# Performance work log

Hardware: AMD Instinct MI355X
Metric: run time of the kernel (lower is better)

## Reference

```python
import jax, jax.numpy as jnp
import numpy as np

N, E, C_IN, C_HID, C_OUT = 50000, 800000, 128, 128, 128


def _mlp2(x, w1, b1, w2, b2):
    # build_mlp: 2 layers, no layer norm, plain_last=False -> ReLU after both
    h = jax.nn.relu(x @ w1 + b1)
    return jax.nn.relu(h @ w2 + b2)


def setup_inputs() -> dict:
    key = jax.random.key(0)
    ks = jax.random.split(key, 16)
    s = 0.05
    inp = {
        "x": jax.random.normal(ks[0], (N, C_IN), jnp.float32),
        "pos": jax.random.normal(ks[1], (N, C_IN), jnp.float32),
        "edge_index": jax.random.randint(ks[2], (2, E), 0, N, jnp.int64),
        # lin_in (with bias)
        "W_in": jax.random.normal(ks[3], (C_IN, C_IN), jnp.float32) * s,
        "b_in": jnp.zeros((C_IN,), jnp.float32),
        # PointTransformerConv linear maps (bias=False in PyG)
        "W_lin": jax.random.normal(ks[4], (C_IN, C_OUT), jnp.float32) * s,
        "W_src": jax.random.normal(ks[5], (C_IN, C_OUT), jnp.float32) * s,
        "W_dst": jax.random.normal(ks[6], (C_IN, C_OUT), jnp.float32) * s,
        # pos_nn: in_channels -> hidden -> out_channels
        "pos_w1": jax.random.normal(ks[7], (C_IN, C_HID), jnp.float32) * s,
        "pos_b1": jnp.zeros((C_HID,), jnp.float32),
        "pos_w2": jax.random.normal(ks[8], (C_HID, C_OUT), jnp.float32) * s,
        "pos_b2": jnp.zeros((C_OUT,), jnp.float32),
        # attn_nn: out_channels -> hidden -> out_channels
        "att_w1": jax.random.normal(ks[9], (C_OUT, C_HID), jnp.float32) * s,
        "att_b1": jnp.zeros((C_HID,), jnp.float32),
        "att_w2": jax.random.normal(ks[10], (C_HID, C_OUT), jnp.float32) * s,
        "att_b2": jnp.zeros((C_OUT,), jnp.float32),
        # lin_out (with bias)
        "W_out": jax.random.normal(ks[11], (C_OUT, C_OUT), jnp.float32) * s,
        "b_out": jnp.zeros((C_OUT,), jnp.float32),
    }
    return inp


def reference(x, pos, edge_index, W_in, b_in, W_lin, W_src, W_dst,
              pos_w1, pos_b1, pos_w2, pos_b2,
              att_w1, att_b1, att_w2, att_b2, W_out, b_out):
    n = x.shape[0]
    src, dst = edge_index[0], edge_index[1]  # j -> i

    h = jax.nn.relu(x @ W_in + b_in)                 # [N, C_IN]
    q = h @ W_dst                                    # dest queries
    k = h @ W_src                                    # source keys
    v = h @ W_lin                                    # values

    delta = _mlp2(pos[dst] - pos[src], pos_w1, pos_b1, pos_w2, pos_b2)  # [E, C_OUT]
    alpha = _mlp2(q[dst] - k[src] + delta, att_w1, att_b1, att_w2, att_b2)

    # per-channel segment softmax over destination nodes
    m = jax.ops.segment_max(alpha, dst, num_segments=n)
    m = jnp.where(jnp.isfinite(m), m, 0.0)
    ea = jnp.exp(alpha - m[dst])
    z = jax.ops.segment_sum(ea, dst, num_segments=n)
    attn = ea / (z[dst] + 1e-16)

    msg = attn * (v[src] + delta)                    # [E, C_OUT]
    agg = jax.ops.segment_sum(msg, dst, num_segments=n)

    return jax.nn.relu(agg @ W_out + b_out)
```

## Files before the change

### kernel.cpp

```cpp
#include <hip/hip_runtime.h>
#include <hip/hip_bf16.h>

#define C 128
#define THREADS 256
#define ETHREADS 128
#define EWPB 2
#define TILE 64
#define EPW 16
#define GTILES 8
#define LDSPAD 8
#define LDSW (C + LDSPAD)
#define LOG2E 1.44269504088896340736f

typedef unsigned short ushortT;
typedef __attribute__((ext_vector_type(8))) short short8;
typedef __attribute__((ext_vector_type(8))) ushortT ushort8;
typedef __attribute__((ext_vector_type(4))) float floatx4;
typedef __attribute__((ext_vector_type(4))) unsigned uintx4;

__device__ __forceinline__ unsigned pk2(float a, float b) {
    float2 f; f.x = a; f.y = b;
    union { unsigned u; __hip_bfloat162 h; } cv; cv.h = __float22bfloat162_rn(f);
    return cv.u;
}
__device__ __forceinline__ ushortT f2bf(float x) {
    return (ushortT)(pk2(x, x) & 0xffffu);
}
__device__ __forceinline__ float bf2f(ushortT h) {
    union { unsigned u; float f; } v; v.u = ((unsigned)h) << 16;
    return v.f;
}
__device__ __forceinline__ float2 upk2(unsigned u) {
    union { unsigned u; __hip_bfloat162 h; } cv; cv.u = u;
    return __bfloat1622float2(cv.h);
}
__device__ __forceinline__ float exp2_hw(float x) {
    float r; asm("v_exp_f32 %0, %1" : "=v"(r) : "v"(x)); return r;
}
__device__ __forceinline__ void atomic_add_f32(float* p, float v) {
    __hip_atomic_fetch_add(p, v, __ATOMIC_RELAXED, __HIP_MEMORY_SCOPE_AGENT);
}

__device__ __forceinline__ void wave_gemm(const ushortT (*A)[LDSW],
                                          const ushortT* __restrict__ Bp,
                                          int quad, int m16, int lane,
                                          floatx4 acc[8])
{
#pragma unroll
    for (int nt = 0; nt < 8; ++nt) { acc[nt][0]=0.f; acc[nt][1]=0.f; acc[nt][2]=0.f; acc[nt][3]=0.f; }
#pragma unroll 1
    for (int ks = 0; ks < 4; ++ks) {
        const short8 af = *(const short8*)&A[m16][ks * 32 + quad * 8];
        const ushortT* bpk = Bp + (size_t)ks * 4096 + (size_t)lane * 8;
#pragma unroll
        for (int nt = 0; nt < 8; ++nt) {
            const short8 bf = *(const short8*)(bpk + nt * 512);
            acc[nt] = __builtin_amdgcn_mfma_f32_16x16x32_bf16(af, bf, acc[nt], 0, 0, 0);
        }
    }
}

__device__ __forceinline__ void cstore_relu_r(ushortT (*A)[LDSW], floatx4 acc[8],
                                              const float bias[8], int quad, int m16)
{
#pragma unroll
    for (int nt = 0; nt < 8; ++nt) {
        const float b = bias[nt];
#pragma unroll
        for (int r = 0; r < 4; r += 2) {
            const unsigned p = pk2(fmaxf(acc[nt][r] + b, 0.f), fmaxf(acc[nt][r + 1] + b, 0.f));
            A[quad * 4 + r][nt * 16 + m16]     = (ushortT)(p & 0xffffu);
            A[quad * 4 + r + 1][nt * 16 + m16] = (ushortT)(p >> 16);
        }
    }
}

__device__ __forceinline__ ushortT pack_one(const float* __restrict__ W, int u) {
    const int j = u & 7, lane = (u >> 3) & 63, f = u >> 9;
    const int nt = f & 7, ks = f >> 3;
    const int n = nt * 16 + (lane & 15);
    const int k = ks * 32 + (lane >> 4) * 8 + j;
    return f2bf(W[k * C + n]);
}

extern "C" __global__ void __launch_bounds__(256)
prep1(const float* __restrict__ pw1, const float* __restrict__ pw2,
      const float* __restrict__ aw1, const float* __restrict__ aw2,
      const float* __restrict__ Wd,  const float* __restrict__ Wsrc,
      const float* __restrict__ Wl,  const float* __restrict__ Win,
      const float* __restrict__ Wout,
      const float* __restrict__ pos, ushortT* __restrict__ pos_bf,
      const int* __restrict__ ei, int* __restrict__ deg,
      ushortT* __restrict__ Bpack, ushortT* __restrict__ Bpack2,
      ushortT* __restrict__ BpackO, int N, int E)
{
    const int nb_cvt = (N * 32 + 255) / 256;
    const int b = blockIdx.x, tid = threadIdx.x;
    if (b < 256) {
        const int t = b * 256 + tid;
        const int s = t >> 14;
        const float* W = (s == 0) ? pw1 : (s == 1) ? pw2 : (s == 2) ? aw1 : aw2;
        const int u = t & 16383;
        const int j = u & 7, lane = (u >> 3) & 63, f = u >> 9;
        const int nt = f & 7, ks = f >> 3;
        const int n = nt * 16 + (lane & 15);
        const int k = ks * 32 + (lane >> 4) * 8 + j;
        float v = W[k * C + n];
        if (s == 3) v *= LOG2E;
        Bpack[t] = f2bf(v);
    } else if (b < 512) {
        const int t = (b - 256) * 256 + tid;
        const int s = t >> 14;
        const float* W = (s == 0) ? Wd : (s == 1) ? Wsrc : (s == 2) ? Wl : Win;
        Bpack2[t] = pack_one(W, t & 16383);
    } else if (b < 576) {
        const int t = (b - 512) * 256 + tid;
        BpackO[t] = pack_one(Wout, t);
    } else if (b < 576 + nb_cvt) {
        const int i = (b - 576) * 256 + tid;
        if (i < N * 32) {
            const float4 v = ((const float4*)pos)[i];
            uint2 o; o.x = pk2(v.x, v.y); o.y = pk2(v.z, v.w);
            ((uint2*)pos_bf)[i] = o;
        }
    } else {
        const int e = (b - 576 - nb_cvt) * 256 + tid;
        if (e < E) atomicAdd(&deg[ei[E + e]], 1);
    }
}

extern "C" __global__ void __launch_bounds__(1024)
k_scan(const int* __restrict__ deg, int* __restrict__ off, int n)
{
    __shared__ int part[1024];
    const int t = threadIdx.x;
    const int chunk = (((n + 1023) / 1024) + 3) & ~3;
    const int lo = t * chunk, hi = min(lo + chunk, n);
    int s = 0;
    for (int i = lo; i < hi; i += 4) {
        const int4 d4 = *(const int4*)(deg + i);
        s += d4.x + d4.y + d4.z + d4.w;
    }
    part[t] = s;
    __syncthreads();
    for (int d = 1; d < 1024; d <<= 1) {
        int v = (t >= d) ? part[t - d] : 0;
        __syncthreads();
        part[t] += v;
        __syncthreads();
    }
    int run = (t == 0) ? 0 : part[t - 1];
    for (int i = lo; i < hi; i += 4) {
        const int4 d4 = *(const int4*)(deg + i);
        int4 o;
        o.x = run;
        o.y = o.x + d4.x;
        o.z = o.y + d4.y;
        o.w = o.z + d4.z;
        *(int4*)(off + i) = o;
        run = o.w + d4.w;
    }
}

extern "C" __global__ void __launch_bounds__(256)
prep2(const float* __restrict__ x, const float* __restrict__ b_in,
      const ushortT* __restrict__ Bp2, const ushortT* __restrict__ Bpk,
      const float* __restrict__ pb1, const ushortT* __restrict__ pos_bf,
      ushortT* __restrict__ q_bf, ushortT* __restrict__ k_bf, ushortT* __restrict__ v_bf,
      ushortT* __restrict__ Pd_arr, ushortT* __restrict__ Ps_arr,
      const int* __restrict__ ei, const int* __restrict__ offp, int* __restrict__ curp,
      int* __restrict__ ss, int* __restrict__ sd, int N, int E, int nb_node)
{
    __shared__ ushortT xs[TILE][LDSW];
    __shared__ ushortT hs[TILE][LDSW];
    const int b = blockIdx.x, tx = threadIdx.x;

    if (b >= nb_node) {
        const int e = (b - nb_node) * 256 + tx;
        if (e < E) {
            const int d = ei[E + e];
            const int p = offp[d] + atomicAdd(&curp[d], 1);
            ss[p] = ei[e];
            sd[p] = d;
        }
        return;
    }

    const int rg = tx >> 5;
    const int oc0 = (tx & 31) << 2;
    const int row0 = b * TILE;

#pragma unroll
    for (int j = 0; j < 8; ++j) {
        const int r = rg * 8 + j, n = row0 + r;
        float4 xv; xv.x = xv.y = xv.z = xv.w = 0.f;
        if (n < N) xv = *(const float4*)(x + (size_t)n * C + oc0);
        *(unsigned*)&xs[r][oc0]     = pk2(xv.x, xv.y);
        *(unsigned*)&xs[r][oc0 + 2] = pk2(xv.z, xv.w);
    }

    const int wv = tx >> 6, lane = tx & 63;
    const int quad = lane >> 4, m16 = lane & 15;
    const int row = lane >> 2, li = lane & 3;

    float binv[8];
#pragma unroll
    for (int nt = 0; nt < 8; ++nt) binv[nt] = b_in[nt * 16 + m16];

    const ushortT (*Ax)[LDSW] = (const ushortT (*)[LDSW])&xs[wv * 16];
    ushortT (*Ah)[LDSW] = (ushortT (*)[LDSW])&hs[wv * 16];

    floatx4 macc[8];
    wave_gemm(Ax, Bp2 + (size_t)3 * 16384, quad, m16, lane, macc);
    cstore_relu_r(Ah, macc, binv, quad, m16);

    __syncthreads();

    ushortT (*OS)[LDSW] = (ushortT (*)[LDSW])&xs[wv * 16];
    ushortT* outs[3];
    outs[0] = q_bf; outs[1] = k_bf; outs[2] = v_bf;

    const int nrow = row0 + wv * 16 + row;

#pragma unroll 1
    for (int m = 0; m < 3; ++m) {
        wave_gemm((const ushortT (*)[LDSW])Ah, Bp2 + (size_t)m * 16384, quad, m16, lane, macc);
#pragma unroll
        for (int nt = 0; nt < 8; ++nt) {
#pragma unroll
            for (int r = 0; r < 4; r += 2) {
                const unsigned p = pk2(macc[nt][r], macc[nt][r + 1]);
                OS[quad * 4 + r][nt * 16 + m16]     = (ushortT)(p & 0xffffu);
                OS[quad * 4 + r + 1][nt * 16 + m16] = (ushortT)(p >> 16);
            }
        }
        if (nrow < N) {
#pragma unroll
            for (int i = 0; i < 4; ++i) {
                const ushort8 v8 = *(const ushort8*)&OS[row][i * 32 + li * 8];
                *(ushort8*)(outs[m] + (size_t)nrow * C + i * 32 + li * 8) = v8;
            }
        }
    }

    __syncthreads();
    {
        const ushortT* srcp = pos_bf + (size_t)min(nrow, N - 1) * C;
#pragma unroll
        for (int i = 0; i < 4; ++i) {
            const ushort8 v8 = *(const ushort8*)(srcp + i * 32 + li * 8);
            *(ushort8*)&hs[wv * 16 + row][i * 32 + li * 8] = v8;
        }
    }
    __syncthreads();
    wave_gemm((const ushortT (*)[LDSW])Ah, Bpk , quad, m16, lane, macc);

    float b1v[8];
#pragma unroll
    for (int nt = 0; nt < 8; ++nt) b1v[nt] = pb1[nt * 16 + m16];

#pragma unroll
    for (int nt = 0; nt < 8; ++nt) {
#pragma unroll
        for (int r = 0; r < 4; r += 2) {
            const unsigned p = pk2(macc[nt][r] + b1v[nt], macc[nt][r + 1] + b1v[nt]);
            OS[quad * 4 + r][nt * 16 + m16]     = (ushortT)(p & 0xffffu);
            OS[quad * 4 + r + 1][nt * 16 + m16] = (ushortT)(p >> 16);
        }
    }
    if (nrow < N) {
#pragma unroll
        for (int i = 0; i < 4; ++i) {
            const ushort8 v8 = *(const ushort8*)&OS[row][i * 32 + li * 8];
            *(ushort8*)(Pd_arr + (size_t)nrow * C + i * 32 + li * 8) = v8;
        }
    }
    __syncthreads();
#pragma unroll
    for (int nt = 0; nt < 8; ++nt) {
#pragma unroll
        for (int r = 0; r < 4; r += 2) {
            const unsigned p = pk2(macc[nt][r], macc[nt][r + 1]);
            OS[quad * 4 + r][nt * 16 + m16]     = (ushortT)(p & 0xffffu);
            OS[quad * 4 + r + 1][nt * 16 + m16] = (ushortT)(p >> 16);
        }
    }
    if (nrow < N) {
#pragma unroll
        for (int i = 0; i < 4; ++i) {
            const ushort8 v8 = *(const ushort8*)&OS[row][i * 32 + li * 8];
            *(ushort8*)(Ps_arr + (size_t)nrow * C + i * 32 + li * 8) = v8;
        }
    }
}

__device__ __forceinline__ void gather4(const ushortT* __restrict__ base, int node, int li,
                                        ushort8 dst[4])
{
    const ushort8* p = (const ushort8*)(base + (size_t)node * C) + li;
    dst[0] = p[0]; dst[1] = p[4]; dst[2] = p[8]; dst[3] = p[12];
}

extern "C" __global__ void __launch_bounds__(ETHREADS)
edge_mfma(const ushortT* __restrict__ Pd_arr, const ushortT* __restrict__ Ps_arr,
          const int* __restrict__ ss, const int* __restrict__ sd,
          const ushortT* __restrict__ q_bf, const ushortT* __restrict__ k_bf,
          const ushortT* __restrict__ v_bf, const ushortT* __restrict__ Bpack,
          const float* __restrict__ pb2,
          const float* __restrict__ ab1, const float* __restrict__ ab2,
          float* __restrict__ z, float* __restrict__ aggU, int E)
{
    __shared__ ushortT Aslab[EWPB][EPW][LDSW];
    __shared__ ushortT Vslab[EWPB][EPW][LDSW];
    __shared__ int     Dslab[EWPB][EPW];
    const int tid = threadIdx.x;
    const int wv = tid >> 6, lane = tid & 63;
    const int quad = lane >> 4, m16 = lane & 15;
    const int row = lane >> 2, li = lane & 3;
    ushortT (*A)[LDSW] = Aslab[wv];
    ushortT (*V)[LDSW] = Vslab[wv];

    float pb2v[8], ab1v[8], ab2v[8];
#pragma unroll
    for (int nt = 0; nt < 8; ++nt) {
        pb2v[nt] = pb2[nt * 16 + m16];
        ab1v[nt] = ab1[nt * 16 + m16];
        ab2v[nt] = ab2[nt * 16 + m16] * LOG2E;
    }

    const ushortT* B1 = Bpack + 16384;
    const ushortT* B2 = Bpack + 32768;
    const ushortT* B3 = Bpack + 49152;

    const int wave_base = (blockIdx.x * EWPB + wv) * (GTILES * EPW);

    const int c2 = lane * 2;
    int   cur_dst = -1;
    float zs0 = 0.f, zs1 = 0.f, gs0 = 0.f, gs1 = 0.f;

    int es, ed, sdr[4];
    {
        const int eidx = min(wave_base + row, E - 1);
        es = ss[eidx]; ed = sd[eidx];
#pragma unroll
        for (int r = 0; r < 4; ++r)
            sdr[r] = sd[min(wave_base + quad * 4 + r, E - 1)];
    }

#pragma unroll 1
    for (int t = 0; t < GTILES; ++t) {
        const int e_base = wave_base + t * EPW;
        if (m16 == 0) {
#pragma unroll
            for (int r = 0; r < 4; ++r) Dslab[wv][quad * 4 + r] = sdr[r];
        }

        ushort8 Pd[4], Ps[4], Qv[4], Kv[4], Vv[4];
        gather4(Pd_arr, ed, li, Pd); gather4(Ps_arr, es, li, Ps);
        gather4(q_bf,  ed, li, Qv); gather4(k_bf,  es, li, Kv);
        gather4(v_bf,  es, li, Vv);

#pragma unroll
        for (int i = 0; i < 4; ++i) {
            const uintx4 pd = *(const uintx4*)&Pd[i];
            const uintx4 ps = *(const uintx4*)&Ps[i];
            uintx4 o;
#pragma unroll
            for (int w = 0; w < 4; ++w) {
                const float2 a = upk2(pd[w]), b = upk2(ps[w]);
                o[w] = pk2(fmaxf(a.x - b.x, 0.f), fmaxf(a.y - b.y, 0.f));
            }
            *(uintx4*)&A[row][i * 32 + li * 8] = o;
            *(ushort8*)&V[row][i * 32 + li * 8] = Vv[i];
        }

        floatx4 acc[8];

        wave_gemm(A, B1, quad, m16, lane, acc);
        unsigned dlp[8][2];
#pragma unroll
        for (int nt = 0; nt < 8; ++nt) {
            const float b = pb2v[nt];
            const unsigned p0 = pk2(fmaxf(acc[nt][0] + b, 0.f), fmaxf(acc[nt][1] + b, 0.f));
            const unsigned p1 = pk2(fmaxf(acc[nt][2] + b, 0.f), fmaxf(acc[nt][3] + b, 0.f));
            dlp[nt][0] = p0; dlp[nt][1] = p1;
            A[quad * 4 + 0][nt * 16 + m16] = (ushortT)(p0 & 0xffffu);
            A[quad * 4 + 1][nt * 16 + m16] = (ushortT)(p0 >> 16);
            A[quad * 4 + 2][nt * 16 + m16] = (ushortT)(p1 & 0xffffu);
            A[quad * 4 + 3][nt * 16 + m16] = (ushortT)(p1 >> 16);
        }

#pragma unroll
        for (int i = 0; i < 4; ++i) {
            const uintx4 dv = *(const uintx4*)&A[row][i * 32 + li * 8];
            const uintx4 qv = *(const uintx4*)&Qv[i];
            const uintx4 kv = *(const uintx4*)&Kv[i];
            uintx4 o;
#pragma unroll
            for (int w = 0; w < 4; ++w) {
                const float2 qq = upk2(qv[w]), kk = upk2(kv[w]), dd = upk2(dv[w]);
                o[w] = pk2(qq.x - kk.x + dd.x, qq.y - kk.y + dd.y);
            }
            *(uintx4*)&A[row][i * 32 + li * 8] = o;
        }

        int nes = es, ned = ed, nsdr[4];
#pragma unroll
        for (int r = 0; r < 4; ++r) nsdr[r] = sdr[r];
        if (t + 1 < GTILES) {
            const int e2 = e_base + EPW;
            const int ei2 = min(e2 + row, E - 1);
            nes = ss[ei2]; ned = sd[ei2];
#pragma unroll
            for (int r = 0; r < 4; ++r)
                nsdr[r] = sd[min(e2 + quad * 4 + r, E - 1)];
        }

        wave_gemm(A, B2, quad, m16, lane, acc);
        cstore_relu_r(A, acc, ab1v, quad, m16);

        wave_gemm(A, B3, quad, m16, lane, acc);
#pragma unroll
        for (int nt = 0; nt < 8; ++nt) {
            const float b = ab2v[nt];
#pragma unroll
            for (int r = 0; r < 4; ++r)
                acc[nt][r] = exp2_hw(fmaxf(acc[nt][r] + b, 0.f));
        }

        if (e_base + EPW > E) {
#pragma unroll
            for (int r = 0; r < 4; ++r)
                if (e_base + quad * 4 + r >= E) {
#pragma unroll
                    for (int nt = 0; nt < 8; ++nt) acc[nt][r] = 0.f;
                }
        }

#pragma unroll
        for (int nt = 0; nt < 8; ++nt) {
#pragma unroll
            for (int r = 0; r < 4; ++r) {
                const float2 dpair = upk2(dlp[nt][r >> 1]);
                const float dlv = (r & 1) ? dpair.y : dpair.x;
                const int ridx = quad * 4 + r, cidx = nt * 16 + m16;
                const float vv = bf2f(V[ridx][cidx]);
                V[ridx][cidx] = f2bf(vv + dlv);
                A[ridx][cidx] = f2bf(acc[nt][r]);
            }
        }

#pragma unroll 4
        for (int e = 0; e < EPW; ++e) {
            const int d = Dslab[wv][e];
            const float2 ea2 = upk2(*(const unsigned*)&A[e][c2]);
            const float2 vp2 = upk2(*(const unsigned*)&V[e][c2]);
            if (d != cur_dst) {
                if (cur_dst >= 0) {
                    float* zp = z    + (size_t)cur_dst * C + c2;
                    float* gp = aggU + (size_t)cur_dst * C + c2;
                    atomic_add_f32(zp,     zs0);
                    atomic_add_f32(zp + 1, zs1);
                    atomic_add_f32(gp,     gs0);
                    atomic_add_f32(gp + 1, gs1);
                }
                cur_dst = d;
                zs0 = ea2.x;           zs1 = ea2.y;
                gs0 = ea2.x * vp2.x;   gs1 = ea2.y * vp2.y;
            } else {
                zs0 += ea2.x;                   zs1 += ea2.y;
                gs0 = fmaf(ea2.x, vp2.x, gs0);  gs1 = fmaf(ea2.y, vp2.y, gs1);
            }
        }

        es = nes; ed = ned;
#pragma unroll
        for (int r = 0; r < 4; ++r) sdr[r] = nsdr[r];
    }

    if (cur_dst >= 0) {
        float* zp = z    + (size_t)cur_dst * C + c2;
        float* gp = aggU + (size_t)cur_dst * C + c2;
        atomic_add_f32(zp,     zs0);
        atomic_add_f32(zp + 1, zs1);
        atomic_add_f32(gp,     gs0);
        atomic_add_f32(gp + 1, gs1);
    }
}

extern "C" __global__ void __launch_bounds__(THREADS)
out_kernel(const float* __restrict__ aggU, const float* __restrict__ z,
           const ushortT* __restrict__ BpO, const float* __restrict__ b_out,
           float* __restrict__ out, int N)
{
    __shared__ ushortT us[TILE][LDSW];
    const int tx = threadIdx.x;
    const int rg = tx >> 5;
    const int oc0 = (tx & 31) << 2;
    const int row0 = blockIdx.x * TILE;

#pragma unroll
    for (int j = 0; j < 8; ++j) {
        const int r = rg * 8 + j, n = row0 + r;
        float4 a; a.x = a.y = a.z = a.w = 0.f;
        if (n < N) {
            const float4 g  = *(const float4*)(aggU + (size_t)n * C + oc0);
            const float4 zz = *(const float4*)(z    + (size_t)n * C + oc0);
            a.x = g.x / (zz.x + 1e-16f);
            a.y = g.y / (zz.y + 1e-16f);
            a.z = g.z / (zz.z + 1e-16f);
            a.w = g.w / (zz.w + 1e-16f);
        }
        *(unsigned*)&us[r][oc0]     = pk2(a.x, a.y);
        *(unsigned*)&us[r][oc0 + 2] = pk2(a.z, a.w);
    }

    const int wv = tx >> 6, lane = tx & 63;
    const int quad = lane >> 4, m16 = lane & 15;

    floatx4 macc[8];
    wave_gemm((const ushortT (*)[LDSW])&us[wv * 16], BpO, quad, m16, lane, macc);

    float bo[8];
#pragma unroll
    for (int nt = 0; nt < 8; ++nt) bo[nt] = b_out[nt * 16 + m16];

#pragma unroll
    for (int r = 0; r < 4; ++r) {
        const int n = row0 + wv * 16 + quad * 4 + r;
        if (n < N) {
            float* op = out + (size_t)n * C + m16;
#pragma unroll
            for (int nt = 0; nt < 8; ++nt)
                op[nt * 16] = fmaxf(macc[nt][r] + bo[nt], 0.f);
        }
    }
}

extern "C" void kernel_launch(void* const* d_in, const int* in_sizes, int n_in,
                              void* d_out, int out_size, void* d_ws, size_t ws_size,
                              hipStream_t stream)
{
    const float* x     = (const float*)d_in[0];
    const float* pos   = (const float*)d_in[1];
    const int*   ei    = (const int*)  d_in[2];
    const float* W_in  = (const float*)d_in[3];
    const float* b_in  = (const float*)d_in[4];
    const float* W_lin = (const float*)d_in[5];
    const float* W_src = (const float*)d_in[6];
    const float* W_dst = (const float*)d_in[7];
    const float* pw1   = (const float*)d_in[8];
    const float* pb1   = (const float*)d_in[9];
    const float* pw2   = (const float*)d_in[10];
    const float* pb2   = (const float*)d_in[11];
    const float* aw1   = (const float*)d_in[12];
    const float* ab1   = (const float*)d_in[13];
    const float* aw2   = (const float*)d_in[14];
    const float* ab2   = (const float*)d_in[15];
    const float* W_out = (const float*)d_in[16];
    const float* b_out = (const float*)d_in[17];

    const int N = in_sizes[0] / C;
    const int E = in_sizes[2] / 2;
    const size_t NC = (size_t)N * C;

    float*   z      = (float*)d_ws;
    float*   aggU   = z + NC;
    ushortT* q_bf   = (ushortT*)(aggU + NC);
    ushortT* k_bf   = q_bf + NC;
    ushortT* v_bf   = k_bf + NC;
    ushortT* Pd_arr = v_bf + NC;
    ushortT* Ps_arr = Pd_arr + NC;
    ushortT* pos_bf = Ps_arr + NC;
    ushortT* Bpack  = pos_bf + NC;
    ushortT* Bpack2 = Bpack + 65536;
    ushortT* BpackO = Bpack2 + 65536;
    int*     deg    = (int*)(BpackO + 16384);
    int*     curp   = deg + N;
    int*     offp   = curp + N;
    int*     ss     = offp + N;
    int*     sdst   = ss + E;

    hipMemsetAsync(z, 0, 2 * NC * sizeof(float), stream);
    hipMemsetAsync(deg, 0, 2 * (size_t)N * sizeof(int), stream);

    const int nb_cvt  = (N * 32 + 255) / 256;
    const int nb_hist = (E + 255) / 256;
    prep1<<<576 + nb_cvt + nb_hist, 256, 0, stream>>>(pw1, pw2, aw1, aw2,
                                                      W_dst, W_src, W_lin, W_in, W_out,
                                                      pos, pos_bf, ei, deg,
                                                      Bpack, Bpack2, BpackO, N, E);

    k_scan<<<1, 1024, 0, stream>>>(deg, offp, N);

    const int nb = (N + TILE - 1) / TILE;
    prep2<<<nb + nb_hist, 256, 0, stream>>>(x, b_in, Bpack2, Bpack, pb1, pos_bf,
                                            q_bf, k_bf, v_bf, Pd_arr, Ps_arr,
                                            ei, offp, curp, ss, sdst, N, E, nb);

    const int edges_per_block = EWPB * GTILES * EPW;
    const int eb = (E + edges_per_block - 1) / edges_per_block;
    edge_mfma<<<eb, ETHREADS, 0, stream>>>(Pd_arr, Ps_arr, ss, sdst, q_bf, k_bf, v_bf, Bpack,
                                           pb2, ab1, ab2, z, aggU, E);
    out_kernel<<<nb, THREADS, 0, stream>>>(aggU, z, BpackO, b_out, (float*)d_out, N);
}
```

Measured before the change: 588.5 us.

## Software-pipeline pos and value gathers one tile ahead in edge kernel

The Pd/Ps/V row gathers for the next 16-edge tile are now issued during the current tile, before the second and third GEMMs, and the edge indices are prefetched two tiles ahead. The aim is to hide gather latency behind MFMA work instead of stalling at the top of each tile. The cost is roughly 48 extra VGPRs held across the loop for the prefetched bf16 rows, which may lower occupancy or cause spills.

```diff
diff --git a/kernel.cpp b/kernel.cpp
--- a/kernel.cpp
+++ b/kernel.cpp
@@ -338,13 +338,24 @@
     int   cur_dst = -1;
     float zs0 = 0.f, zs1 = 0.f, gs0 = 0.f, gs1 = 0.f;
 
-    int es, ed, sdr[4];
+    int esC, edC, sdrC[4];
+    int esN, edN, sdrN[4];
+    ushort8 PdP[4], PsP[4], VvP[4];
     {
         const int eidx = min(wave_base + row, E - 1);
-        es = ss[eidx]; ed = sd[eidx];
+        esC = ss[eidx]; edC = sd[eidx];
 #pragma unroll
         for (int r = 0; r < 4; ++r)
-            sdr[r] = sd[min(wave_base + quad * 4 + r, E - 1)];
+            sdrC[r] = sd[min(wave_base + quad * 4 + r, E - 1)];
+        gather4(Pd_arr, edC, li, PdP);
+        gather4(Ps_arr, esC, li, PsP);
+        gather4(v_bf,  esC, li, VvP);
+        const int e2 = wave_base + EPW;
+        const int ei2 = min(e2 + row, E - 1);
+        esN = ss[ei2]; edN = sd[ei2];
+#pragma unroll
+        for (int r = 0; r < 4; ++r)
+            sdrN[r] = sd[min(e2 + quad * 4 + r, E - 1)];
     }
 
 #pragma unroll 1
@@ -352,18 +363,17 @@
         const int e_base = wave_base + t * EPW;
         if (m16 == 0) {
 #pragma unroll
-            for (int r = 0; r < 4; ++r) Dslab[wv][quad * 4 + r] = sdr[r];
-        }
-
-        ushort8 Pd[4], Ps[4], Qv[4], Kv[4], Vv[4];
-        gather4(Pd_arr, ed, li, Pd); gather4(Ps_arr, es, li, Ps);
-        gather4(q_bf,  ed, li, Qv); gather4(k_bf,  es, li, Kv);
-        gather4(v_bf,  es, li, Vv);
+            for (int r = 0; r < 4; ++r) Dslab[wv][quad * 4 + r] = sdrC[r];
+        }
+
+        ushort8 Qv[4], Kv[4];
+        gather4(q_bf, edC, li, Qv);
+        gather4(k_bf, esC, li, Kv);
 
 #pragma unroll
         for (int i = 0; i < 4; ++i) {
-            const uintx4 pd = *(const uintx4*)&Pd[i];
-            const uintx4 ps = *(const uintx4*)&Ps[i];
+            const uintx4 pd = *(const uintx4*)&PdP[i];
+            const uintx4 ps = *(const uintx4*)&PsP[i];
             uintx4 o;
 #pragma unroll
             for (int w = 0; w < 4; ++w) {
@@ -371,7 +381,7 @@
                 o[w] = pk2(fmaxf(a.x - b.x, 0.f), fmaxf(a.y - b.y, 0.f));
             }
             *(uintx4*)&A[row][i * 32 + li * 8] = o;
-            *(ushort8*)&V[row][i * 32 + li * 8] = Vv[i];
+            *(ushort8*)&V[row][i * 32 + li * 8] = VvP[i];
         }
 
         floatx4 acc[8];
@@ -404,16 +414,22 @@
             *(uintx4*)&A[row][i * 32 + li * 8] = o;
         }
 
-        int nes = es, ned = ed, nsdr[4];
-#pragma unroll
-        for (int r = 0; r < 4; ++r) nsdr[r] = sdr[r];
+        ushort8 PdN[4], PsN[4], VvN[4];
         if (t + 1 < GTILES) {
-            const int e2 = e_base + EPW;
+            gather4(Pd_arr, edN, li, PdN);
+            gather4(Ps_arr, esN, li, PsN);
+            gather4(v_bf,  esN, li, VvN);
+        }
+        int esN2 = esN, edN2 = edN, nsdr2[4];
+#pragma unroll
+        for (int r = 0; r < 4; ++r) nsdr2[r] = sdrN[r];
+        if (t + 2 < GTILES) {
+            const int e2 = e_base + 2 * EPW;
             const int ei2 = min(e2 + row, E - 1);
-            nes = ss[ei2]; ned = sd[ei2];
+            esN2 = ss[ei2]; edN2 = sd[ei2];
 #pragma unroll
             for (int r = 0; r < 4; ++r)
-                nsdr[r] = sd[min(e2 + quad * 4 + r, E - 1)];
+                nsdr2[r] = sd[min(e2 + quad * 4 + r, E - 1)];
         }
 
         wave_gemm(A, B2, quad, m16, lane, acc);
@@ -473,9 +489,14 @@
             }
         }
 
-        es = nes; ed = ned;
-#pragma unroll
-        for (int r = 0; r < 4; ++r) sdr[r] = nsdr[r];
+        esC = esN; edC = edN;
+#pragma unroll
+        for (int r = 0; r < 4; ++r) sdrC[r] = sdrN[r];
+        esN = esN2; edN = edN2;
+#pragma unroll
+        for (int r = 0; r < 4; ++r) sdrN[r] = nsdr2[r];
+#pragma unroll
+        for (int i = 0; i < 4; ++i) { PdP[i] = PdN[i]; PsP[i] = PsN[i]; VvP[i] = VvN[i]; }
     }
 
     if (cur_dst >= 0) {
```

After: 602.8 us. 2.4% more time.
